# Kernel optimization log

Measured on AMD Instinct MI355X. Metric: run time of the kernel, lower is better.

## Reference

```python
import jax, jax.numpy as jnp
import numpy as np

N_CAM, N_REF, N_HEADS, EMBD = 6, 4, 8, 256
OUT = 10
L = OUT * OUT            # seq_len = output_size^2
HS = EMBD // N_HEADS
BS = 2


def setup_inputs() -> dict:
    key = jax.random.key(0)
    k1, k2, k3 = jax.random.split(key, 3)
    # C'*H'*W' must equal seq_len*embd = 100*256 = 25600 -> (256,10,10)
    single_frame_feature = jax.random.normal(k1, (BS, 1, N_CAM, 256, 10, 10), jnp.float32)
    bev_query = jax.random.normal(k2, (BS, L, EMBD), jnp.float32)
    W_v = jax.random.normal(k3, (N_CAM * EMBD, N_REF * EMBD), jnp.float32) / np.float32(np.sqrt(N_CAM * EMBD))
    b_v = jnp.zeros((N_REF * EMBD,), jnp.float32)
    return {"single_frame_feature": single_frame_feature, "bev_query": bev_query, "W_v": W_v, "b_v": b_v}


def reference(single_frame_feature, bev_query, W_v, b_v):
    bs, _, n_cam, C, H, W = single_frame_feature.shape
    _, seq_len, embd = bev_query.shape
    nh, hs, n_ref = N_HEADS, embd // N_HEADS, N_REF
    R = n_cam * n_ref  # repeat factor

    # (bs, n_cam, seq_len, embd) -- C*H*W == seq_len*embd by construction
    feat = single_frame_feature.reshape(bs, n_cam, seq_len, embd)

    # q: (bs, seq_len, nh, hs) repeated over cameras x ref points -> (bs, R*L, nh, hs)
    q = bev_query.reshape(bs, seq_len, nh, hs)
    q = jnp.tile(q, (1, R, 1, 1))

    # k: camera features broadcast over ref points, ordered (cam, ref, L)
    k = feat.reshape(bs, n_cam, 1, seq_len, nh, hs)
    k = jnp.broadcast_to(k, (bs, n_cam, n_ref, seq_len, nh, hs)).reshape(bs, R * seq_len, nh, hs)

    # v: per-location linear mixing cameras into n_ref value slots (self.v)
    v_in = feat.transpose(0, 2, 1, 3).reshape(bs, seq_len, n_cam * embd)
    v = v_in @ W_v + b_v                                   # (bs, L, n_ref*embd)
    v = v.reshape(bs, seq_len, n_ref, nh, hs).transpose(0, 2, 1, 3, 4)  # (bs, n_ref, L, nh, hs)
    v = jnp.broadcast_to(v[:, None], (bs, n_cam, n_ref, seq_len, nh, hs)).reshape(bs, R * seq_len, nh, hs)

    # scaled dot-product attention (dropout is identity at eval)
    scores = jnp.einsum('bqhd,bkhd->bhqk', q, k) / jnp.sqrt(jnp.float32(hs))
    att = jax.nn.softmax(scores, axis=-1)                  # (bs, nh, R*L, R*L)
    out = jnp.einsum('bhqk,bkhd->bqhd', att, v)            # (bs, R*L, nh, hs)

    # fold the R repeated views back to the BEV grid (uniform ref weights)
    out = out.reshape(bs, R, seq_len, embd).mean(axis=1)   # (bs, L, embd)
    return out
```

## Files before the change

### kernel.cpp

```cpp
#include <hip/hip_runtime.h>

#define N_CAM   6
#define N_REF   4
#define N_HEADS 8
#define EMBD    256
#define HS      32
#define L       100
#define BS      2
#define CAM_STRIDE (L * EMBD)
#define CK      (N_CAM * L)

#define WS_WSUM 0
#define WS_KTR  (WS_WSUM + 1536*256)
#define WS_P    (WS_KTR + 307200)
#define WS_VSUM (WS_P + 12*200*256)
#define WS_E    (WS_VSUM + 51200)

__global__ __launch_bounds__(256) void prep_kernel(const float* __restrict__ feat,
                                                   const float4* __restrict__ Wv4,
                                                   float* __restrict__ ws) {
    const int t = threadIdx.x;
    if (blockIdx.x < 96) {
        __shared__ float tile[100][33];
        int blk = blockIdx.x;
        int b   = blk / 48;
        int rem = blk - b * 48;
        int cam = rem >> 3;
        int h   = rem & 7;
        const float* src = feat + (size_t)(b * N_CAM + cam) * CAM_STRIDE + h * HS;
        for (int idx = t; idx < 100 * 32; idx += 256) {
            int sk = idx >> 5;
            int d  = idx & 31;
            tile[sk][d] = src[sk * EMBD + d];
        }
        __syncthreads();
        float* ktr = ws + WS_KTR;
        for (int idx = t; idx < 100 * 32; idx += 256) {
            int d  = idx / 100;
            int sk = idx - d * 100;
            ktr[((size_t)(b * N_HEADS + h) * HS + d) * CK + cam * L + sk] = tile[sk][d];
        }
    } else {
        int tid = (blockIdx.x - 96) * 256 + t;
        int i  = tid >> 6;
        int e4 = tid & 63;
        const float4* row = Wv4 + (size_t)i * 256;
        float4 a = row[e4];
        float4 b = row[64 + e4];
        float4 c = row[128 + e4];
        float4 d = row[192 + e4];
        float4 o;
        o.x = a.x + b.x + c.x + d.x;
        o.y = a.y + b.y + c.y + d.y;
        o.z = a.z + b.z + c.z + d.z;
        o.w = a.w + b.w + c.w + d.w;
        ((float4*)(ws + WS_WSUM))[(size_t)i * 64 + e4] = o;
    }
}

__global__ __launch_bounds__(256) void vsum_gemm_kernel(const float* __restrict__ feat,
                                                        const float* __restrict__ ws_in,
                                                        float* __restrict__ ws_out) {
    __shared__ float a_tile[4][128];
    const int t  = threadIdx.x;
    const int rg = blockIdx.x / 12;
    const int c  = blockIdx.x - rg * 12;
    const int r0 = rg * 4;
    const int k0 = c * 128;
    const int cam    = c >> 1;
    const int e2base = (c & 1) << 7;

    for (int idx = t; idx < 4 * 128; idx += 256) {
        int j  = idx >> 7;
        int kk = idx & 127;
        int row = r0 + j;
        int b = row >= 100;
        int s = row - b * 100;
        a_tile[j][kk] = feat[(size_t)(b * N_CAM + cam) * CAM_STRIDE + s * EMBD + e2base + kk];
    }
    __syncthreads();

    float acc[4] = {0.f, 0.f, 0.f, 0.f};
    const float* wp = ws_in + WS_WSUM + (size_t)k0 * 256 + t;
#pragma unroll 8
    for (int kk = 0; kk < 128; ++kk) {
        float w = wp[kk * 256];
#pragma unroll
        for (int j = 0; j < 4; ++j) acc[j] += a_tile[j][kk] * w;
    }

    float* P = ws_out + WS_P;
#pragma unroll
    for (int j = 0; j < 4; ++j)
        P[((size_t)c * 200 + r0 + j) * 256 + t] = acc[j];
}

__global__ __launch_bounds__(256) void mid_kernel(const float* __restrict__ query,
                                                  const float* __restrict__ b_v,
                                                  float* __restrict__ ws) {
    const int t = threadIdx.x;
    if (blockIdx.x < 200) {
        const int row = blockIdx.x;
        const float* P = ws + WS_P;
        float acc = b_v[t] + b_v[256 + t] + b_v[512 + t] + b_v[768 + t];
#pragma unroll
        for (int c = 0; c < 12; ++c)
            acc += P[((size_t)c * 200 + row) * 256 + t];
        ws[WS_VSUM + (size_t)row * 256 + t] = acc;
    } else {
        __shared__ float q_s[4][32];
        __shared__ float es[4][CK];
        int idx = blockIdx.x - 200;
        int b   = idx / 200;
        int rem = idx - b * 200;
        int h   = rem / 25;
        int sqt = rem - h * 25;
        int sq0 = sqt * 4;

        if (t < 128) {
            int sqj = t >> 5;
            int d   = t & 31;
            q_s[sqj][d] = query[(size_t)(b * L + sq0 + sqj) * EMBD + h * HS + d];
        }
        __syncthreads();

        const float scale = 0.17677669529663687f;
        const float* kt = ws + WS_KTR + (size_t)(b * N_HEADS + h) * HS * CK;

#pragma unroll
        for (int i = 0; i < 3; ++i) {
            int ck = t + i * 256;
            if (ck < CK) {
                float acc0 = 0.f, acc1 = 0.f, acc2 = 0.f, acc3 = 0.f;
#pragma unroll 8
                for (int d = 0; d < 32; ++d) {
                    float k = kt[(size_t)d * CK + ck];
                    acc0 += q_s[0][d] * k;
                    acc1 += q_s[1][d] * k;
                    acc2 += q_s[2][d] * k;
                    acc3 += q_s[3][d] * k;
                }
                es[0][ck] = __expf(acc0 * scale);
                es[1][ck] = __expf(acc1 * scale);
                es[2][ck] = __expf(acc2 * scale);
                es[3][ck] = __expf(acc3 * scale);
            }
        }
        __syncthreads();

        float* E = ws + WS_E;
        for (int p = t; p < 4 * L; p += 256) {
            int sqj = p / 100;
            int sk  = p - sqj * 100;
            float e = 0.f;
#pragma unroll
            for (int cam = 0; cam < N_CAM; ++cam)
                e += es[sqj][cam * L + sk];
            E[((size_t)(b * L + sq0 + sqj) * N_HEADS + h) * L + sk] = e;
        }
    }
}

__global__ __launch_bounds__(256) void out_kernel(const float* __restrict__ ws,
                                                  float* __restrict__ out) {
    const int t  = threadIdx.x;
    const int b  = blockIdx.x / 100;
    const int sq = blockIdx.x - b * 100;
    const int h  = t >> 5;

    const float* Eh = ws + WS_E + ((size_t)(b * L + sq) * N_HEADS + h) * L;
    const float* vb = ws + WS_VSUM + (size_t)b * L * EMBD + t;

    float acc = 0.f, sumE = 0.f;
#pragma unroll 4
    for (int sk = 0; sk < L; ++sk) {
        float e = Eh[sk];
        acc  += e * vb[sk * EMBD];
        sumE += e;
    }
    out[(size_t)(b * L + sq) * EMBD + t] = acc * (0.25f / sumE);
}

extern "C" void kernel_launch(void* const* d_in, const int* in_sizes, int n_in,
                              void* d_out, int out_size, void* d_ws, size_t ws_size,
                              hipStream_t stream) {
    const float* feat  = (const float*)d_in[0];
    const float* query = (const float*)d_in[1];
    const float* Wv    = (const float*)d_in[2];
    const float* bv    = (const float*)d_in[3];
    float* outp = (float*)d_out;
    float* ws   = (float*)d_ws;

    prep_kernel<<<480, 256, 0, stream>>>(feat, (const float4*)Wv, ws);

    vsum_gemm_kernel<<<600, 256, 0, stream>>>(feat, ws, ws);

    mid_kernel<<<600, 256, 0, stream>>>(query, bv, ws);

    out_kernel<<<200, 256, 0, stream>>>(ws, outp);
}
```

Before: 93.58 us.

## Fuse four kernels into one cooperative kernel with grid-wide syncs

After: 310.4 us. 3.32x slower.

```diff
diff --git a/kernel.cpp b/kernel.cpp
--- a/kernel.cpp
+++ b/kernel.cpp
@@ -1,4 +1,7 @@
 #include <hip/hip_runtime.h>
+#include <hip/hip_cooperative_groups.h>
+
+namespace cg = cooperative_groups;
 
 #define N_CAM   6
 #define N_REF   4
@@ -16,13 +19,20 @@
 #define WS_VSUM (WS_P + 12*200*256)
 #define WS_E    (WS_VSUM + 51200)
 
-__global__ __launch_bounds__(256) void prep_kernel(const float* __restrict__ feat,
-                                                   const float4* __restrict__ Wv4,
-                                                   float* __restrict__ ws) {
-    const int t = threadIdx.x;
-    if (blockIdx.x < 96) {
-        __shared__ float tile[100][33];
-        int blk = blockIdx.x;
+#define NBLK 600
+
+__global__ __launch_bounds__(256, 4) void fused_kernel(const float* __restrict__ feat,
+                                                       const float* __restrict__ query,
+                                                       const float4* __restrict__ Wv4,
+                                                       const float* __restrict__ b_v,
+                                                       float* __restrict__ ws,
+                                                       float* __restrict__ out) {
+    cg::grid_group grid = cg::this_grid();
+    __shared__ float smem[100 * 33];
+    const int t   = threadIdx.x;
+    const int blk = blockIdx.x;
+
+    if (blk < 96) {
         int b   = blk / 48;
         int rem = blk - b * 48;
         int cam = rem >> 3;
@@ -31,76 +41,73 @@
         for (int idx = t; idx < 100 * 32; idx += 256) {
             int sk = idx >> 5;
             int d  = idx & 31;
-            tile[sk][d] = src[sk * EMBD + d];
+            smem[sk * 33 + d] = src[sk * EMBD + d];
         }
         __syncthreads();
         float* ktr = ws + WS_KTR;
         for (int idx = t; idx < 100 * 32; idx += 256) {
             int d  = idx / 100;
             int sk = idx - d * 100;
-            ktr[((size_t)(b * N_HEADS + h) * HS + d) * CK + cam * L + sk] = tile[sk][d];
+            ktr[((size_t)(b * N_HEADS + h) * HS + d) * CK + cam * L + sk] = smem[sk * 33 + d];
         }
     } else {
-        int tid = (blockIdx.x - 96) * 256 + t;
-        int i  = tid >> 6;
-        int e4 = tid & 63;
-        const float4* row = Wv4 + (size_t)i * 256;
-        float4 a = row[e4];
-        float4 b = row[64 + e4];
-        float4 c = row[128 + e4];
-        float4 d = row[192 + e4];
-        float4 o;
-        o.x = a.x + b.x + c.x + d.x;
-        o.y = a.y + b.y + c.y + d.y;
-        o.z = a.z + b.z + c.z + d.z;
-        o.w = a.w + b.w + c.w + d.w;
-        ((float4*)(ws + WS_WSUM))[(size_t)i * 64 + e4] = o;
-    }
-}
-
-__global__ __launch_bounds__(256) void vsum_gemm_kernel(const float* __restrict__ feat,
-                                                        const float* __restrict__ ws_in,
-                                                        float* __restrict__ ws_out) {
-    __shared__ float a_tile[4][128];
-    const int t  = threadIdx.x;
-    const int rg = blockIdx.x / 12;
-    const int c  = blockIdx.x - rg * 12;
-    const int r0 = rg * 4;
-    const int k0 = c * 128;
-    const int cam    = c >> 1;
-    const int e2base = (c & 1) << 7;
-
-    for (int idx = t; idx < 4 * 128; idx += 256) {
-        int j  = idx >> 7;
-        int kk = idx & 127;
-        int row = r0 + j;
-        int b = row >= 100;
-        int s = row - b * 100;
-        a_tile[j][kk] = feat[(size_t)(b * N_CAM + cam) * CAM_STRIDE + s * EMBD + e2base + kk];
-    }
-    __syncthreads();
-
-    float acc[4] = {0.f, 0.f, 0.f, 0.f};
-    const float* wp = ws_in + WS_WSUM + (size_t)k0 * 256 + t;
+        int tid = (blk - 96) * 256 + t;
+        if (tid < 1536 * 64) {
+            int i  = tid >> 6;
+            int e4 = tid & 63;
+            const float4* row = Wv4 + (size_t)i * 256;
+            float4 a = row[e4];
+            float4 b = row[64 + e4];
+            float4 c = row[128 + e4];
+            float4 d = row[192 + e4];
+            float4 o;
+            o.x = a.x + b.x + c.x + d.x;
+            o.y = a.y + b.y + c.y + d.y;
+            o.z = a.z + b.z + c.z + d.z;
+            o.w = a.w + b.w + c.w + d.w;
+            ((float4*)(ws + WS_WSUM))[(size_t)i * 64 + e4] = o;
+        }
+    }
+    grid.sync();
+
+    {
+        const int rg = blk / 12;
+        const int c  = blk - rg * 12;
+        const int r0 = rg * 4;
+        const int k0 = c * 128;
+        const int cam    = c >> 1;
+        const int e2base = (c & 1) << 7;
+
+        float* a_tile = smem;
+        for (int idx = t; idx < 4 * 128; idx += 256) {
+            int j  = idx >> 7;
+            int kk = idx & 127;
+            int row = r0 + j;
+            int b = row >= 100;
+            int s = row - b * 100;
+            a_tile[j * 128 + kk] =
+                feat[(size_t)(b * N_CAM + cam) * CAM_STRIDE + s * EMBD + e2base + kk];
+        }
+        __syncthreads();
+
+        float acc[4] = {0.f, 0.f, 0.f, 0.f};
+        const float* wp = ws + WS_WSUM + (size_t)k0 * 256 + t;
 #pragma unroll 8
-    for (int kk = 0; kk < 128; ++kk) {
-        float w = wp[kk * 256];
-#pragma unroll
-        for (int j = 0; j < 4; ++j) acc[j] += a_tile[j][kk] * w;
-    }
-
-    float* P = ws_out + WS_P;
-#pragma unroll
-    for (int j = 0; j < 4; ++j)
-        P[((size_t)c * 200 + r0 + j) * 256 + t] = acc[j];
-}
-
-__global__ __launch_bounds__(256) void mid_kernel(const float* __restrict__ query,
-                                                  const float* __restrict__ b_v,
-                                                  float* __restrict__ ws) {
-    const int t = threadIdx.x;
-    if (blockIdx.x < 200) {
-        const int row = blockIdx.x;
+        for (int kk = 0; kk < 128; ++kk) {
+            float w = wp[kk * 256];
+#pragma unroll
+            for (int j = 0; j < 4; ++j) acc[j] += a_tile[j * 128 + kk] * w;
+        }
+
+        float* P = ws + WS_P;
+#pragma unroll
+        for (int j = 0; j < 4; ++j)
+            P[((size_t)c * 200 + r0 + j) * 256 + t] = acc[j];
+    }
+    grid.sync();
+
+    if (blk < 200) {
+        const int row = blk;
         const float* P = ws + WS_P;
         float acc = b_v[t] + b_v[256 + t] + b_v[512 + t] + b_v[768 + t];
 #pragma unroll
@@ -108,9 +115,9 @@
             acc += P[((size_t)c * 200 + row) * 256 + t];
         ws[WS_VSUM + (size_t)row * 256 + t] = acc;
     } else {
-        __shared__ float q_s[4][32];
-        __shared__ float es[4][CK];
-        int idx = blockIdx.x - 200;
+        float* q_s = smem;
+        float* es  = smem + 128;
+        int idx = blk - 200;
         int b   = idx / 200;
         int rem = idx - b * 200;
         int h   = rem / 25;
@@ -120,7 +127,7 @@
         if (t < 128) {
             int sqj = t >> 5;
             int d   = t & 31;
-            q_s[sqj][d] = query[(size_t)(b * L + sq0 + sqj) * EMBD + h * HS + d];
+            q_s[sqj * 32 + d] = query[(size_t)(b * L + sq0 + sqj) * EMBD + h * HS + d];
         }
         __syncthreads();
 
@@ -135,15 +142,15 @@
 #pragma unroll 8
                 for (int d = 0; d < 32; ++d) {
                     float k = kt[(size_t)d * CK + ck];
-                    acc0 += q_s[0][d] * k;
-                    acc1 += q_s[1][d] * k;
-                    acc2 += q_s[2][d] * k;
-                    acc3 += q_s[3][d] * k;
+                    acc0 += q_s[0 * 32 + d] * k;
+                    acc1 += q_s[1 * 32 + d] * k;
+                    acc2 += q_s[2 * 32 + d] * k;
+                    acc3 += q_s[3 * 32 + d] * k;
                 }
-                es[0][ck] = __expf(acc0 * scale);
-                es[1][ck] = __expf(acc1 * scale);
-                es[2][ck] = __expf(acc2 * scale);
-                es[3][ck] = __expf(acc3 * scale);
+                es[0 * CK + ck] = __expf(acc0 * scale);
+                es[1 * CK + ck] = __expf(acc1 * scale);
+                es[2 * CK + ck] = __expf(acc2 * scale);
+                es[3 * CK + ck] = __expf(acc3 * scale);
             }
         }
         __syncthreads();
@@ -155,30 +162,29 @@
             float e = 0.f;
 #pragma unroll
             for (int cam = 0; cam < N_CAM; ++cam)
-                e += es[sqj][cam * L + sk];
+                e += es[sqj * CK + cam * L + sk];
             E[((size_t)(b * L + sq0 + sqj) * N_HEADS + h) * L + sk] = e;
         }
     }
-}
-
-__global__ __launch_bounds__(256) void out_kernel(const float* __restrict__ ws,
-                                                  float* __restrict__ out) {
-    const int t  = threadIdx.x;
-    const int b  = blockIdx.x / 100;
-    const int sq = blockIdx.x - b * 100;
-    const int h  = t >> 5;
-
-    const float* Eh = ws + WS_E + ((size_t)(b * L + sq) * N_HEADS + h) * L;
-    const float* vb = ws + WS_VSUM + (size_t)b * L * EMBD + t;
-
-    float acc = 0.f, sumE = 0.f;
+    grid.sync();
+
+    if (blk < 200) {
+        const int b  = blk / 100;
+        const int sq = blk - b * 100;
+        const int h  = t >> 5;
+
+        const float* Eh = ws + WS_E + ((size_t)(b * L + sq) * N_HEADS + h) * L;
+        const float* vb = ws + WS_VSUM + (size_t)b * L * EMBD + t;
+
+        float acc = 0.f, sumE = 0.f;
 #pragma unroll 4
-    for (int sk = 0; sk < L; ++sk) {
-        float e = Eh[sk];
-        acc  += e * vb[sk * EMBD];
-        sumE += e;
-    }
-    out[(size_t)(b * L + sq) * EMBD + t] = acc * (0.25f / sumE);
+        for (int sk = 0; sk < L; ++sk) {
+            float e = Eh[sk];
+            acc  += e * vb[sk * EMBD];
+            sumE += e;
+        }
+        out[(size_t)(b * L + sq) * EMBD + t] = acc * (0.25f / sumE);
+    }
 }
 
 extern "C" void kernel_launch(void* const* d_in, const int* in_sizes, int n_in,
@@ -186,16 +192,13 @@
                               hipStream_t stream) {
     const float* feat  = (const float*)d_in[0];
     const float* query = (const float*)d_in[1];
-    const float* Wv    = (const float*)d_in[2];
+    const float4* Wv   = (const float4*)d_in[2];
     const float* bv    = (const float*)d_in[3];
     float* outp = (float*)d_out;
     float* ws   = (float*)d_ws;
 
-    prep_kernel<<<480, 256, 0, stream>>>(feat, (const float4*)Wv, ws);
-
-    vsum_gemm_kernel<<<600, 256, 0, stream>>>(feat, ws, ws);
-
-    mid_kernel<<<600, 256, 0, stream>>>(query, bv, ws);
-
-    out_kernel<<<200, 256, 0, stream>>>(ws, outp);
+    void* args[] = {(void*)&feat, (void*)&query, (void*)&Wv,
+                    (void*)&bv,   (void*)&ws,    (void*)&outp};
+    hipLaunchCooperativeKernel((void*)fused_kernel, dim3(NBLK), dim3(256),
+                               args, 0, stream);
 }
```
